# Kernel optimization log

Measured on AMD Instinct MI355X. Metric: run time of the kernel, lower is better.

The kernel has to match this reference:

```python
import jax, jax.numpy as jnp
import numpy as np

ALPHA = 0.2  # LeakyReLU negative slope
EPS = 1e-6


def gam(x):
    # relu6(x+3)/3 + eps
    return jnp.clip(x + 3.0, 0.0, 6.0) / 3.0 + EPS


def leaky(x):
    return jnp.where(x >= 0, x, ALPHA * x)


def relu_bt(x):
    # threshold at detached inf-norm of input: min(leaky_relu(x), ||x||_inf)
    t = jax.lax.stop_gradient(jnp.max(jnp.abs(x)))
    return jnp.minimum(leaky(x), t)


def setup_inputs() -> dict:
    key = jax.random.key(0)
    ks = jax.random.split(key, 8)
    N, E, Din, Dout = 100000, 1600000, 256, 64
    return {
        "input": jax.random.normal(ks[0], (N, Din), dtype=jnp.float32),
        "edge": jax.random.randint(ks[1], (2, E), 0, N, dtype=jnp.int32),
        "W_high": jax.random.normal(ks[2], (Din, Dout), dtype=jnp.float32) * 0.06,
        "W_low": jax.random.normal(ks[3], (Din, Dout), dtype=jnp.float32) * 0.06,
        "a_high": jax.random.normal(ks[4], (1, 4 * Dout), dtype=jnp.float32) * 0.09,
        "a_low": jax.random.normal(ks[5], (1, 4 * Dout), dtype=jnp.float32) * 0.09,
        "c_high": jax.random.uniform(ks[6], (1, 1), dtype=jnp.float32),
        "c_low": jax.random.uniform(ks[7], (1, 1), dtype=jnp.float32),
    }


def reference(input, edge, W_high, W_low, a_high, a_low, c_high, c_low):
    N = input.shape[0]
    F = W_high.shape[1]
    src, dst = edge[0], edge[1]

    theta_high = gam(c_high) / 2.0  # [1,1]
    theta_low = gam(c_low) / 2.0

    h_high = relu_bt(input @ W_high)  # [N,F]
    h_low = relu_bt(input @ W_low)

    hh_s, hh_d = h_high[src], h_high[dst]  # [E,F]
    hl_s, hl_d = h_low[src], h_low[dst]

    ah = a_high[0]
    al = a_low[0]
    # a . [h_i, h_j, h_i+h_j, h_i-h_j] folded into per-endpoint coefficients
    # NOTE: original code uses h_high for the first two blocks of the LOW branch too.
    score_high = hh_s @ (ah[:F] + ah[2 * F:3 * F] + ah[3 * F:]) \
               + hh_d @ (ah[F:2 * F] + ah[2 * F:3 * F] - ah[3 * F:])  # [E]
    score_low = hh_s @ al[:F] + hh_d @ al[F:2 * F] \
              + hl_s @ (al[2 * F:3 * F] + al[3 * F:]) \
              + hl_d @ (al[2 * F:3 * F] - al[3 * F:])

    e_high = jnp.exp(-leaky(score_high / jnp.linalg.norm(a_high)))  # [E]
    e_low = jnp.exp(-leaky(score_low / jnp.linalg.norm(a_low)))

    # sparse COO spmm: rowsum and weighted aggregation
    rowsum_high = jax.ops.segment_sum(e_high, src, num_segments=N)[:, None]  # [N,1]
    rowsum_low = jax.ops.segment_sum(e_low, src, num_segments=N)[:, None]
    hp_high = jax.ops.segment_sum(e_high[:, None] * hh_d, src, num_segments=N)  # [N,F]
    hp_low = jax.ops.segment_sum(e_low[:, None] * hl_d, src, num_segments=N)

    hp_high = hp_high / (rowsum_high + theta_high)
    hp_low = hp_low / (rowsum_low + theta_low)

    # concat=True branch
    return relu_bt(jnp.concatenate([hp_high, hp_low], axis=1))  # [N,2F]
```

## Files before the change

kernel.cpp:

```cpp
#include <hip/hip_runtime.h>
#include <hip/hip_bf16.h>
#include <hip/hip_fp16.h>
#include <math.h>

typedef unsigned short ushort_t;
typedef unsigned int uint_t;
typedef __attribute__((ext_vector_type(8))) short short8;
typedef __attribute__((ext_vector_type(4))) float floatx4;
typedef __attribute__((ext_vector_type(4))) uint_t uintx4;

#define ALPHA 0.2f
#define CAP 64
#define NXCD 8

__device__ __forceinline__ float leaky(float x) { return x >= 0.0f ? x : ALPHA * x; }

__device__ __forceinline__ float bf2f(ushort_t u) {
    union { uint_t i; float f; } v; v.i = ((uint_t)u) << 16; return v.f;
}
__device__ __forceinline__ ushort_t f2bf(float f) {
    union { float f; uint_t i; } v; v.f = f;
    return (ushort_t)((v.i + 0x8000u) >> 16);
}
__device__ __forceinline__ uint_t pack_bf2(float a, float b) {
    union { float f; uint_t i; } ua, ub; ua.f = a; ub.f = b;
    return ((ua.i + 0x8000u) >> 16) | ((ub.i + 0x8000u) & 0xffff0000u);
}

__global__ void prep_wtrans_kernel(const float* __restrict__ Wh, const float* __restrict__ Wl,
                                   ushort_t* __restrict__ WTg,
                                   const float* __restrict__ ah, const float* __restrict__ al,
                                   const float* __restrict__ ch, const float* __restrict__ cl,
                                   float* __restrict__ coef, float* __restrict__ consts) {
    int t = threadIdx.x;
    if (blockIdx.x < 128) {
        int c = blockIdx.x;
        float v = (c < 64) ? Wh[t * 64 + c] : Wl[t * 64 + (c - 64)];
        WTg[c * 256 + t] = f2bf(v);
        return;
    }
    __shared__ float red[256];
    float va = ah[t];
    red[t] = va * va;
    __syncthreads();
    for (int s = 128; s > 0; s >>= 1) { if (t < s) red[t] += red[t + s]; __syncthreads(); }
    float sum_h = red[0];
    __syncthreads();
    float vb = al[t];
    red[t] = vb * vb;
    __syncthreads();
    for (int s = 128; s > 0; s >>= 1) { if (t < s) red[t] += red[t + s]; __syncthreads(); }
    float sum_l = red[0];

    if (t == 0) {
        consts[0] = 1.0f / sqrtf(sum_h);
        consts[1] = 1.0f / sqrtf(sum_l);
        float c = ch[0];
        float g = fminf(fmaxf(c + 3.0f, 0.0f), 6.0f) / 3.0f + 1e-6f;
        consts[2] = g * 0.5f;
        c = cl[0];
        g = fminf(fmaxf(c + 3.0f, 0.0f), 6.0f) / 3.0f + 1e-6f;
        consts[3] = g * 0.5f;
    }
    if (t < 128) {
        int f = t;
        float c0, c1, c2, c3;
        if (f < 64) {
            c0 = ah[f] + ah[128 + f] + ah[192 + f];
            c1 = ah[64 + f] + ah[128 + f] - ah[192 + f];
            c2 = al[f];
            c3 = al[64 + f];
        } else {
            int g = f - 64;
            c0 = 0.0f;
            c1 = 0.0f;
            c2 = al[128 + g] + al[192 + g];
            c3 = al[128 + g] - al[192 + g];
        }
        coef[0 * 128 + f] = c0;
        coef[1 * 128 + f] = c1;
        coef[2 * 128 + f] = c2;
        coef[3 * 128 + f] = c3;
    }
}

__global__ __launch_bounds__(256, 4) void gemm_kernel(const float* __restrict__ in,
                                                      const ushort_t* __restrict__ WTg,
                                                      const float* __restrict__ coef,
                                                      ushort_t* __restrict__ hcat,
                                                      float* __restrict__ s4, int N) {
    __shared__ ushort_t WT[128 * 128];
    __shared__ float coefS[512];
    int tid = threadIdx.x;
    for (int i = tid; i < 512; i += 256) coefS[i] = coef[i];

    int wave = tid >> 6, lane = tid & 63;
    int quad = lane >> 4, m16 = lane & 15;
    int rowbase = blockIdx.x * 64 + wave * 16;
    int arow = rowbase + m16;
    if (arow >= N) arow = N - 1;

    floatx4 acc[8];
#pragma unroll
    for (int ct = 0; ct < 8; ++ct) acc[ct] = (floatx4){0.0f, 0.0f, 0.0f, 0.0f};

    const uint4* WTg4 = (const uint4*)WTg;

#pragma unroll
    for (int kh = 0; kh < 2; ++kh) {
        if (kh) __syncthreads();
        for (int i = tid; i < 2048; i += 256) {
            int c = i >> 4, j = i & 15;
            int sj = j ^ (c & 7);
            uint4 v = WTg4[c * 32 + kh * 16 + j];
            *(uint4*)&WT[c * 128 + sj * 8] = v;
        }
        __syncthreads();
#pragma unroll
        for (int ks = 0; ks < 4; ++ks) {
            const float* ap = in + (size_t)arow * 256 + kh * 128 + ks * 32 + quad * 8;
            float4 a0 = *(const float4*)ap;
            float4 a1 = *(const float4*)(ap + 4);
            union { uintx4 u; short8 s; } av;
            av.u[0] = pack_bf2(a0.x, a0.y);
            av.u[1] = pack_bf2(a0.z, a0.w);
            av.u[2] = pack_bf2(a1.x, a1.y);
            av.u[3] = pack_bf2(a1.z, a1.w);
#pragma unroll
            for (int ct = 0; ct < 8; ++ct) {
                int c = ct * 16 + m16;
                int sch = (ks * 4 + quad) ^ (c & 7);
                short8 b = *(const short8*)&WT[c * 128 + sch * 8];
                acc[ct] = __builtin_amdgcn_mfma_f32_16x16x32_bf16(av.s, b, acc[ct], 0, 0, 0);
            }
        }
    }

    float hv[8][4];
#pragma unroll
    for (int ct = 0; ct < 8; ++ct) {
#pragma unroll
        for (int r = 0; r < 4; ++r) {
            int row = rowbase + quad * 4 + r;
            float v = leaky(acc[ct][r]);
            hv[ct][r] = v;
            if (row < N) hcat[(size_t)row * 128 + ct * 16 + m16] = f2bf(v);
        }
    }
#pragma unroll
    for (int r = 0; r < 4; ++r) {
        int row = rowbase + quad * 4 + r;
        float p0 = 0, p1 = 0, p2 = 0, p3 = 0;
#pragma unroll
        for (int ct = 0; ct < 8; ++ct) {
            int c = ct * 16 + m16;
            float h = hv[ct][r];
            p0 += coefS[c] * h;
            p1 += coefS[128 + c] * h;
            p2 += coefS[256 + c] * h;
            p3 += coefS[384 + c] * h;
        }
#pragma unroll
        for (int off = 1; off < 16; off <<= 1) {
            p0 += __shfl_xor(p0, off);
            p1 += __shfl_xor(p1, off);
            p2 += __shfl_xor(p2, off);
            p3 += __shfl_xor(p3, off);
        }
        if (m16 == 0 && row < N) {
            floatx4 v = {p0, p1, p2, p3};
            *(floatx4*)&s4[(size_t)row * 4] = v;
        }
    }
}

__global__ __launch_bounds__(256) void scatter_kernel(const int* __restrict__ edge,
                                                      int* __restrict__ cursor,
                                                      uint_t* __restrict__ elist,
                                                      int E, int N) {
    int xcd = blockIdx.x & (NXCD - 1);
    int chunk = blockIdx.x >> 3;
    int nchunks = gridDim.x >> 3;
    int TN = (N + NXCD - 1) / NXCD;
    int lo = xcd * TN;
    int hiN = lo + TN;
    int stride = nchunks * 256;
    for (int e = chunk * 256 + threadIdx.x; e < E; e += stride) {
        int src = edge[e];
        if (src >= lo && src < hiN) {
            int dst = edge[E + e];
            int pos = atomicAdd(&cursor[src], 1);
            if (pos < CAP) elist[(size_t)src * CAP + pos] = (uint_t)dst;
        }
    }
}

__global__ __launch_bounds__(256) void aggregate_kernel(const int* __restrict__ deg,
                                                        const uint_t* __restrict__ elist,
                                                        const ushort_t* __restrict__ hcat,
                                                        const float* __restrict__ s4,
                                                        const float* __restrict__ consts,
                                                        float* __restrict__ out, int N) {
    int w = (blockIdx.x * blockDim.x + threadIdx.x) >> 6;
    int lane = threadIdx.x & 63;
    if (w >= N) return;
    int d = deg[w];
    if (d > CAP) d = CAP;
    int s = w * CAP;
    int e = s + d;
    bool hi = lane < 32;
    int col = lane * 2;

    float inv_norm = hi ? consts[0] : consts[1];
    float s_own = s4[(size_t)w * 4 + (hi ? 0 : 2)];
    const float* s4o = s4 + (hi ? 1 : 3);

    float a0 = 0, a1 = 0, b0 = 0, b1 = 0;
    float sw0 = 0, sw1 = 0;

    int i = s;
    for (; i + 8 <= e; i += 8) {
        uint_t rr[8];
#pragma unroll
        for (int j = 0; j < 8; ++j) rr[j] = elist[i + j];
        uint_t pp[8];
        float so[8];
#pragma unroll
        for (int j = 0; j < 8; ++j) {
            so[j] = s4o[(size_t)rr[j] * 4];
            pp[j] = *(const uint_t*)&hcat[(size_t)rr[j] * 128 + col];
        }
#pragma unroll
        for (int j = 0; j < 8; ++j) {
            float wt = __expf(-leaky((s_own + so[j]) * inv_norm));
            float f0 = bf2f((ushort_t)(pp[j] & 0xffff));
            float f1 = bf2f((ushort_t)(pp[j] >> 16));
            if (j & 1) { b0 += wt * f0; b1 += wt * f1; sw1 += wt; }
            else       { a0 += wt * f0; a1 += wt * f1; sw0 += wt; }
        }
    }
    for (; i < e; ++i) {
        uint_t rec = elist[i];
        float so = s4o[(size_t)rec * 4];
        uint_t p = *(const uint_t*)&hcat[(size_t)rec * 128 + col];
        float wt = __expf(-leaky((s_own + so) * inv_norm));
        a0 += wt * bf2f((ushort_t)(p & 0xffff));
        a1 += wt * bf2f((ushort_t)(p >> 16));
        sw0 += wt;
    }

    float acc0 = a0 + b0;
    float acc1 = a1 + b1;
    float rsum = sw0 + sw1;

    float theta = hi ? consts[2] : consts[3];
    float inv = 1.0f / (rsum + theta);
    float2 r;
    r.x = leaky(acc0 * inv);
    r.y = leaky(acc1 * inv);
    *(float2*)&out[(size_t)w * 128 + col] = r;
}

extern "C" void kernel_launch(void* const* d_in, const int* in_sizes, int n_in,
                              void* d_out, int out_size, void* d_ws, size_t ws_size,
                              hipStream_t stream) {
    const float* input = (const float*)d_in[0];
    const int* edge = (const int*)d_in[1];
    const float* Wh = (const float*)d_in[2];
    const float* Wl = (const float*)d_in[3];
    const float* ah = (const float*)d_in[4];
    const float* al = (const float*)d_in[5];
    const float* ch = (const float*)d_in[6];
    const float* cl = (const float*)d_in[7];
    int N = in_sizes[0] / 256;
    int E = in_sizes[1] / 2;
    float* out = (float*)d_out;

    char* ws = (char*)d_ws;
    size_t off = 0;
    uint_t* elist = (uint_t*)(ws + off);     off += (size_t)N * CAP * 4;
    ushort_t* hcat = (ushort_t*)(ws + off);  off += (size_t)N * 128 * 2;
    float* s4 = (float*)(ws + off);          off += (size_t)N * 4 * 4;
    int* cursor = (int*)(ws + off);          off += (size_t)N * 4;
    ushort_t* WTg = (ushort_t*)(ws + off);   off += 128 * 256 * 2;
    float* coef = (float*)(ws + off);        off += 4 * 128 * 4;
    float* consts = (float*)(ws + off);      off += 64;

    hipMemsetAsync(cursor, 0, (size_t)N * 4, stream);
    prep_wtrans_kernel<<<129, 256, 0, stream>>>(Wh, Wl, WTg, ah, al, ch, cl, coef, consts);
    gemm_kernel<<<(N + 63) / 64, 256, 0, stream>>>(input, WTg, coef, hcat, s4, N);
    int nchunks = (E + 256 * 8 - 1) / (256 * 8);
    scatter_kernel<<<nchunks * NXCD, 256, 0, stream>>>(edge, cursor, elist, E, N);
    aggregate_kernel<<<(N + 3) / 4, 256, 0, stream>>>(cursor, elist, hcat, s4, consts, out, N);
}
```

Baseline: 369.1 us.

## Compute edge weights lane-parallel once per edge and broadcast via shuffles

```diff
diff --git a/kernel.cpp b/kernel.cpp
--- a/kernel.cpp
+++ b/kernel.cpp
@@ -17,6 +17,12 @@
 
 __device__ __forceinline__ float bf2f(ushort_t u) {
     union { uint_t i; float f; } v; v.i = ((uint_t)u) << 16; return v.f;
+}
+__device__ __forceinline__ float bflo(uint_t p) {
+    union { uint_t i; float f; } v; v.i = p << 16; return v.f;
+}
+__device__ __forceinline__ float bfhi(uint_t p) {
+    union { uint_t i; float f; } v; v.i = p & 0xffff0000u; return v.f;
 }
 __device__ __forceinline__ ushort_t f2bf(float f) {
     union { float f; uint_t i; } v; v.f = f;
@@ -206,59 +212,73 @@
     if (w >= N) return;
     int d = deg[w];
     if (d > CAP) d = CAP;
-    int s = w * CAP;
-    int e = s + d;
+
+    float s_own_h = s4[(size_t)w * 4 + 0];
+    float s_own_l = s4[(size_t)w * 4 + 2];
+    float inv_h = consts[0], inv_l = consts[1];
+    int dst = 0;
+    float wh = 0.0f, wl = 0.0f;
+    if (lane < d) {
+        dst = (int)elist[(size_t)w * CAP + lane];
+        float4 sv = *(const float4*)&s4[(size_t)dst * 4];
+        wh = __expf(-leaky((s_own_h + sv.y) * inv_h));
+        wl = __expf(-leaky((s_own_l + sv.w) * inv_l));
+    }
+    uint_t wp = (uint_t)__half_as_ushort(__float2half(wh))
+              | ((uint_t)__half_as_ushort(__float2half(wl)) << 16);
+    float rsh = wh, rsl = wl;
+#pragma unroll
+    for (int off = 1; off < 64; off <<= 1) {
+        rsh += __shfl_xor(rsh, off);
+        rsl += __shfl_xor(rsl, off);
+    }
+
     bool hi = lane < 32;
-    int col = lane * 2;
-
-    float inv_norm = hi ? consts[0] : consts[1];
-    float s_own = s4[(size_t)w * 4 + (hi ? 0 : 2)];
-    const float* s4o = s4 + (hi ? 1 : 3);
+    int wsh = hi ? 0 : 16;
+    const ushort_t* hbase = hcat + lane * 2;
 
     float a0 = 0, a1 = 0, b0 = 0, b1 = 0;
-    float sw0 = 0, sw1 = 0;
-
-    int i = s;
-    for (; i + 8 <= e; i += 8) {
-        uint_t rr[8];
-#pragma unroll
-        for (int j = 0; j < 8; ++j) rr[j] = elist[i + j];
-        uint_t pp[8];
-        float so[8];
-#pragma unroll
-        for (int j = 0; j < 8; ++j) {
-            so[j] = s4o[(size_t)rr[j] * 4];
-            pp[j] = *(const uint_t*)&hcat[(size_t)rr[j] * 128 + col];
-        }
-#pragma unroll
-        for (int j = 0; j < 8; ++j) {
-            float wt = __expf(-leaky((s_own + so[j]) * inv_norm));
-            float f0 = bf2f((ushort_t)(pp[j] & 0xffff));
-            float f1 = bf2f((ushort_t)(pp[j] >> 16));
-            if (j & 1) { b0 += wt * f0; b1 += wt * f1; sw1 += wt; }
-            else       { a0 += wt * f0; a1 += wt * f1; sw0 += wt; }
-        }
-    }
-    for (; i < e; ++i) {
-        uint_t rec = elist[i];
-        float so = s4o[(size_t)rec * 4];
-        uint_t p = *(const uint_t*)&hcat[(size_t)rec * 128 + col];
-        float wt = __expf(-leaky((s_own + so) * inv_norm));
-        a0 += wt * bf2f((ushort_t)(p & 0xffff));
-        a1 += wt * bf2f((ushort_t)(p >> 16));
-        sw0 += wt;
+    int j = 0;
+    for (; j + 4 <= d; j += 4) {
+        int d0 = __shfl(dst, j);
+        int d1 = __shfl(dst, j + 1);
+        int d2 = __shfl(dst, j + 2);
+        int d3 = __shfl(dst, j + 3);
+        uint_t u0 = (uint_t)__shfl((int)wp, j);
+        uint_t u1 = (uint_t)__shfl((int)wp, j + 1);
+        uint_t u2 = (uint_t)__shfl((int)wp, j + 2);
+        uint_t u3 = (uint_t)__shfl((int)wp, j + 3);
+        uint_t p0 = *(const uint_t*)&hbase[(size_t)d0 * 128];
+        uint_t p1 = *(const uint_t*)&hbase[(size_t)d1 * 128];
+        uint_t p2 = *(const uint_t*)&hbase[(size_t)d2 * 128];
+        uint_t p3 = *(const uint_t*)&hbase[(size_t)d3 * 128];
+        float w0 = __half2float(__ushort_as_half((ushort_t)(u0 >> wsh)));
+        float w1 = __half2float(__ushort_as_half((ushort_t)(u1 >> wsh)));
+        float w2 = __half2float(__ushort_as_half((ushort_t)(u2 >> wsh)));
+        float w3 = __half2float(__ushort_as_half((ushort_t)(u3 >> wsh)));
+        a0 += w0 * bflo(p0); a1 += w0 * bfhi(p0);
+        b0 += w1 * bflo(p1); b1 += w1 * bfhi(p1);
+        a0 += w2 * bflo(p2); a1 += w2 * bfhi(p2);
+        b0 += w3 * bflo(p3); b1 += w3 * bfhi(p3);
+    }
+    for (; j < d; ++j) {
+        int dj = __shfl(dst, j);
+        uint_t uj = (uint_t)__shfl((int)wp, j);
+        uint_t p = *(const uint_t*)&hbase[(size_t)dj * 128];
+        float wt = __half2float(__ushort_as_half((ushort_t)(uj >> wsh)));
+        a0 += wt * bflo(p);
+        a1 += wt * bfhi(p);
     }
 
     float acc0 = a0 + b0;
     float acc1 = a1 + b1;
-    float rsum = sw0 + sw1;
-
+    float rsum = hi ? rsh : rsl;
     float theta = hi ? consts[2] : consts[3];
     float inv = 1.0f / (rsum + theta);
     float2 r;
     r.x = leaky(acc0 * inv);
     r.y = leaky(acc1 * inv);
-    *(float2*)&out[(size_t)w * 128 + col] = r;
+    *(float2*)&out[(size_t)w * 128 + lane * 2] = r;
 }
 
 extern "C" void kernel_launch(void* const* d_in, const int* in_sizes, int n_in,
```

Result: faster. 356.5 us (-3.4%).
